# Kernel optimization log

Measured on AMD Instinct MI355X. Metric: run time of the kernel, lower is better.

Reference implementation:

```python
import jax, jax.numpy as jnp
import numpy as np

N = 100000
E = 1600000
F_IN = 256
H1, C1 = 8, 8          # conv1: 8 heads x 8 channels -> 64
H2, C2 = 1, 32         # conv2: 1 head x num_classes
SLOPE = 0.2


def gat_conv(x, src, dst, n, W, a_src, a_dst, b, heads, out):
    # x: [n, f_in]; W: [f_in, heads*out]; a_src/a_dst: [heads, out]; b: [heads*out]
    h = (x @ W).reshape(n, heads, out)                       # [n, H, C]
    s = jnp.sum(h * a_src, axis=-1)                          # [n, H]
    d = jnp.sum(h * a_dst, axis=-1)                          # [n, H]
    e = jax.nn.leaky_relu(s[src] + d[dst], SLOPE)            # [e, H]
    m = jax.ops.segment_max(e, dst, num_segments=n)          # stable segment softmax
    ex = jnp.exp(e - m[dst])
    z = jax.ops.segment_sum(ex, dst, num_segments=n)
    alpha = ex / (z[dst] + 1e-16)                            # [e, H]
    msg = alpha[:, :, None] * h[src]                         # [e, H, C]
    agg = jax.ops.segment_sum(msg, dst, num_segments=n)      # [n, H, C]
    return agg.reshape(n, heads * out) + b


def setup_inputs() -> dict:
    key = jax.random.key(0)
    ks = jax.random.split(key, 10)
    x = jax.random.normal(ks[0], (N, F_IN), dtype=jnp.float32)
    edge_index = jax.random.randint(ks[1], (2, E), 0, N, dtype=jnp.int32)
    sc = 0.05
    W1 = jax.random.normal(ks[2], (F_IN, H1 * C1), dtype=jnp.float32) * sc
    att_src1 = jax.random.normal(ks[3], (H1, C1), dtype=jnp.float32) * sc
    att_dst1 = jax.random.normal(ks[4], (H1, C1), dtype=jnp.float32) * sc
    b1 = jnp.zeros((H1 * C1,), dtype=jnp.float32)
    W2 = jax.random.normal(ks[5], (H1 * C1, H2 * C2), dtype=jnp.float32) * sc
    att_src2 = jax.random.normal(ks[6], (H2, C2), dtype=jnp.float32) * sc
    att_dst2 = jax.random.normal(ks[7], (H2, C2), dtype=jnp.float32) * sc
    b2 = jnp.zeros((H2 * C2,), dtype=jnp.float32)
    return {"x": x, "edge_index": edge_index, "W1": W1, "att_src1": att_src1,
            "att_dst1": att_dst1, "b1": b1, "W2": W2, "att_src2": att_src2,
            "att_dst2": att_dst2, "b2": b2}


def reference(x, edge_index, W1, att_src1, att_dst1, b1, W2, att_src2, att_dst2, b2):
    # add self loops (PyG GATConv default)
    loops = jnp.arange(N, dtype=edge_index.dtype)
    src = jnp.concatenate([edge_index[0], loops])
    dst = jnp.concatenate([edge_index[1], loops])
    # dropout layers are identity in eval mode
    h = gat_conv(x, src, dst, N, W1, att_src1, att_dst1, b1, H1, C1)
    h = jax.nn.elu(h)
    h = gat_conv(h, src, dst, N, W2, att_src2, att_dst2, b2, H2, C2)
    return jax.nn.log_softmax(h, axis=1)
```

## Files before the change

### kernel.cpp

```cpp
#include <hip/hip_runtime.h>
#include <hip/hip_bf16.h>

#define N_NODES 100000
#define N_EDGES 1600000
#define N_TOT   (N_EDGES + N_NODES)
#define F_IN    256
#define F1      64
#define H1      8
#define C1      8
#define F2      32
#define SLOPE   0.2f
#define CHUNK   2048
#define NCH     ((N_NODES + CHUNK - 1) / CHUNK)

#define NB_G    ((N_NODES + 255) / 256)
#define NB_H    ((N_EDGES + 255) / 256)

#define SLICES  8
#define SL_W    ((N_NODES + SLICES - 1) / SLICES)
#define CH_E    16384
#define NCHUNK  ((N_EDGES + CH_E - 1) / CH_E)

typedef unsigned int  uint;
typedef unsigned short ushort;
typedef __attribute__((ext_vector_type(8))) short bf16x8;
typedef __attribute__((ext_vector_type(4))) float f32x4;

__device__ inline ushort f2bf(float f) {
    uint u = __float_as_uint(f);
    uint r = u + 0x7fffu + ((u >> 16) & 1u);
    return (ushort)(r >> 16);
}
__device__ inline float bflo(uint u) { return __uint_as_float(u << 16); }
__device__ inline float bfhi(uint u) { return __uint_as_float(u & 0xffff0000u); }
__device__ inline uint pk2bf(float a, float b) {
    __hip_bfloat162 h = __float22bfloat162_rn(make_float2(a, b));
    union { __hip_bfloat162 h; uint u; } cv; cv.h = h;
    return cv.u;
}

__global__ __launch_bounds__(256) void k_gemm1_hist(
        const float* __restrict__ x, const float* __restrict__ W1,
        const float* __restrict__ as1, const float* __restrict__ ad1,
        const int* __restrict__ ei,
        ushort* __restrict__ h1b, float* __restrict__ s1, float* __restrict__ d1,
        int* __restrict__ cnt, int* __restrict__ rank) {
    __shared__ union {
        ushort B[F_IN * F1];
        ushort S[4][64][66];
    } sm;
    const int tid = threadIdx.x;

    if (blockIdx.x >= NB_G) {
        const int e = (blockIdx.x - NB_G) * 256 + tid;
        if (e < N_EDGES)
            rank[e] = atomicAdd(cnt + ei[N_EDGES + e], 1);
        return;
    }

    for (int i = 0; i < 64; ++i) {
        const int e = i * 256 + tid;
        const int k = e >> 6, n = e & 63;
        sm.B[((k >> 3) * 64 + n) * 8 + (k & 7)] = f2bf(W1[e]);
    }
    __syncthreads();

    const int wave = tid >> 6, lane = tid & 63;
    const int q = lane >> 4, ln = lane & 15;
    const int rowbase = blockIdx.x * 256 + wave * 64;

    f32x4 acc[4][4];
#pragma unroll
    for (int mt = 0; mt < 4; ++mt)
#pragma unroll
        for (int nt = 0; nt < 4; ++nt) acc[mt][nt] = (f32x4){0.f, 0.f, 0.f, 0.f};

    int rows[4];
#pragma unroll
    for (int mt = 0; mt < 4; ++mt) {
        const int r = rowbase + mt * 16 + ln;
        rows[mt] = r < N_NODES ? r : N_NODES - 1;
    }

    for (int t = 0; t < 8; ++t) {
        bf16x8 bfr[4];
#pragma unroll
        for (int nt = 0; nt < 4; ++nt)
            bfr[nt] = *(const bf16x8*)&sm.B[((t * 4 + q) * 64 + nt * 16 + ln) * 8];
#pragma unroll
        for (int mt = 0; mt < 4; ++mt) {
            const float4* ap = (const float4*)(x + (size_t)rows[mt] * F_IN + t * 32 + q * 8);
            const float4 a0 = ap[0], a1 = ap[1];
            uint4 au = make_uint4(pk2bf(a0.x, a0.y), pk2bf(a0.z, a0.w),
                                  pk2bf(a1.x, a1.y), pk2bf(a1.z, a1.w));
            bf16x8 af = *(bf16x8*)&au;
#pragma unroll
            for (int nt = 0; nt < 4; ++nt)
                acc[mt][nt] = __builtin_amdgcn_mfma_f32_16x16x32_bf16(
                                  af, bfr[nt], acc[mt][nt], 0, 0, 0);
        }
    }
    __syncthreads();

#pragma unroll
    for (int mt = 0; mt < 4; ++mt)
#pragma unroll
        for (int nt = 0; nt < 4; ++nt)
#pragma unroll
            for (int r = 0; r < 4; ++r)
                sm.S[wave][mt * 16 + q * 4 + r][nt * 16 + ln] = f2bf(acc[mt][nt][r]);
    __syncthreads();

    const int node = rowbase + lane;
    if (node >= N_NODES) return;
    const uint* srow = (const uint*)&sm.S[wave][lane][0];
    float sacc[H1], dacc[H1];
#pragma unroll
    for (int h = 0; h < H1; ++h) { sacc[h] = 0.f; dacc[h] = 0.f; }
    uint4* hout = (uint4*)(h1b + (size_t)node * F1);
#pragma unroll
    for (int p4 = 0; p4 < 8; ++p4) {
        const uint u0 = srow[p4 * 4 + 0], u1 = srow[p4 * 4 + 1];
        const uint u2 = srow[p4 * 4 + 2], u3 = srow[p4 * 4 + 3];
        hout[p4] = make_uint4(u0, u1, u2, u3);
        const float c[8] = {bflo(u0), bfhi(u0), bflo(u1), bfhi(u1),
                            bflo(u2), bfhi(u2), bflo(u3), bfhi(u3)};
#pragma unroll
        for (int j = 0; j < 8; ++j) {
            sacc[p4] += c[j] * as1[p4 * 8 + j];
            dacc[p4] += c[j] * ad1[p4 * 8 + j];
        }
    }
    float4* s4 = (float4*)(s1 + (size_t)node * H1);
    float4* d4 = (float4*)(d1 + (size_t)node * H1);
    s4[0] = make_float4(sacc[0], sacc[1], sacc[2], sacc[3]);
    s4[1] = make_float4(sacc[4], sacc[5], sacc[6], sacc[7]);
    d4[0] = make_float4(dacc[0], dacc[1], dacc[2], dacc[3]);
    d4[1] = make_float4(dacc[4], dacc[5], dacc[6], dacc[7]);
}

__global__ __launch_bounds__(256) void k_scan_a(
        const int* __restrict__ cnt, int* __restrict__ row_ptr,
        int* __restrict__ bsum) {
    __shared__ int sdata[256];
    const int tid = threadIdx.x;
    const int base = blockIdx.x * CHUNK + tid * 8;
    int v[8];
    int tot = 0;
#pragma unroll
    for (int j = 0; j < 8; ++j) {
        v[j] = (base + j < N_NODES) ? cnt[base + j] + 1 : 0;
        tot += v[j];
    }
    sdata[tid] = tot;
    __syncthreads();
    for (int off = 1; off < 256; off <<= 1) {
        int t = (tid >= off) ? sdata[tid - off] : 0;
        __syncthreads();
        sdata[tid] += t;
        __syncthreads();
    }
    int run = sdata[tid] - tot;
#pragma unroll
    for (int j = 0; j < 8; ++j) {
        if (base + j < N_NODES) row_ptr[base + j] = run;
        run += v[j];
    }
    if (tid == 255) bsum[blockIdx.x] = sdata[255];
}

__global__ __launch_bounds__(256) void k_scan_c2(
        int* __restrict__ row_ptr, const int* __restrict__ bsum,
        int* __restrict__ srcs) {
    __shared__ int pb[64];
    const int t = threadIdx.x;
    if (t < 64) {
        int v = (t < NCH) ? bsum[t] : 0;
        const int orig = v;
        for (int off = 1; off < 64; off <<= 1) {
            int u = __shfl_up(v, off);
            if (t >= off) v += u;
        }
        pb[t] = v - orig;
    }
    __syncthreads();
    const int i = blockIdx.x * 256 + t;
    if (i < N_NODES) {
        const int rp = row_ptr[i] + pb[i / CHUNK];
        row_ptr[i] = rp;
        srcs[rp] = i;
    } else if (i == N_NODES) row_ptr[N_NODES] = N_TOT;
}

__global__ __launch_bounds__(256) void k_scatter(
        const int* __restrict__ ei, const int* __restrict__ row_ptr,
        const int* __restrict__ rank, int* __restrict__ srcs) {
    const int slice = blockIdx.x % SLICES;
    const int chunk = blockIdx.x / SLICES;
    const int lo = slice * SL_W;
    const int base = chunk * CH_E;
    const int lim = (base + CH_E < N_EDGES) ? base + CH_E : N_EDGES;
    for (int i = base + threadIdx.x; i < lim; i += 256) {
        const int di = ei[N_EDGES + i];
        if ((uint)(di - lo) < (uint)SL_W)
            srcs[row_ptr[di] + 1 + rank[i]] = ei[i];
    }
}

__global__ __launch_bounds__(256) void k_agg1(
        const int* __restrict__ row_ptr, const int* __restrict__ srcs,
        const ushort* __restrict__ h1b, const float* __restrict__ s1,
        const float* __restrict__ d1, const float* __restrict__ b1,
        ushort* __restrict__ x2b) {
    const int wid = (blockIdx.x * 256 + threadIdx.x) >> 6;
    if (wid >= N_NODES) return;
    const int lane = threadIdx.x & 63;
    const int q = lane >> 4;
    const int c = lane & 15;
    const int hd = c >> 1;
    const float dh = d1[(size_t)wid * H1 + hd];
    const int beg = row_ptr[wid], end = row_ptr[wid + 1];
    const uint2* hv = (const uint2*)h1b;
    float a0 = 0.f, a1 = 0.f, a2 = 0.f, a3 = 0.f, z = 0.f;
    int i = beg + q;
    for (; i + 4 < end; i += 8) {
        const int sA = srcs[i], sB = srcs[i + 4];
        float eA = s1[(size_t)sA * H1 + hd] + dh;
        float eB = s1[(size_t)sB * H1 + hd] + dh;
        eA = eA > 0.f ? eA : SLOPE * eA;
        eB = eB > 0.f ? eB : SLOPE * eB;
        const float xA = __expf(eA), xB = __expf(eB);
        const uint2 UA = hv[(size_t)sA * 16 + c];
        const uint2 UB = hv[(size_t)sB * 16 + c];
        z  += xA + xB;
        a0 += xA * bflo(UA.x) + xB * bflo(UB.x);
        a1 += xA * bfhi(UA.x) + xB * bfhi(UB.x);
        a2 += xA * bflo(UA.y) + xB * bflo(UB.y);
        a3 += xA * bfhi(UA.y) + xB * bfhi(UB.y);
    }
    for (; i < end; i += 4) {
        const int sA = srcs[i];
        float eA = s1[(size_t)sA * H1 + hd] + dh;
        eA = eA > 0.f ? eA : SLOPE * eA;
        const float xA = __expf(eA);
        const uint2 UA = hv[(size_t)sA * 16 + c];
        z  += xA;
        a0 += xA * bflo(UA.x);
        a1 += xA * bfhi(UA.x);
        a2 += xA * bflo(UA.y);
        a3 += xA * bfhi(UA.y);
    }
#pragma unroll
    for (int off = 16; off <= 32; off <<= 1) {
        a0 += __shfl_xor(a0, off); a1 += __shfl_xor(a1, off);
        a2 += __shfl_xor(a2, off); a3 += __shfl_xor(a3, off);
        z  += __shfl_xor(z, off);
    }
    if (lane < 16) {
        const float zi = 1.f / (z + 1e-16f);
        float v0 = a0 * zi + b1[4 * c + 0];
        float v1 = a1 * zi + b1[4 * c + 1];
        float v2 = a2 * zi + b1[4 * c + 2];
        float v3 = a3 * zi + b1[4 * c + 3];
        v0 = v0 > 0.f ? v0 : __expf(v0) - 1.f;
        v1 = v1 > 0.f ? v1 : __expf(v1) - 1.f;
        v2 = v2 > 0.f ? v2 : __expf(v2) - 1.f;
        v3 = v3 > 0.f ? v3 : __expf(v3) - 1.f;
        ((uint2*)x2b)[(size_t)wid * 16 + c] = make_uint2(pk2bf(v0, v1), pk2bf(v2, v3));
    }
}

__global__ __launch_bounds__(256) void k_node1(
        const ushort* __restrict__ x2b, const float* __restrict__ W2,
        const float* __restrict__ as2, const float* __restrict__ ad2,
        ushort* __restrict__ h2b, float* __restrict__ s2, float* __restrict__ d2) {
    __shared__ float sW[F1 * F2];
    const int tid = threadIdx.x;
    const float4* W4 = (const float4*)W2;
    float4* sW4 = (float4*)sW;
#pragma unroll
    for (int i = 0; i < (F1 * F2 / 4) / 256; ++i)
        sW4[i * 256 + tid] = W4[i * 256 + tid];
    __syncthreads();

    const int n = blockIdx.x * 256 + tid;
    if (n >= N_NODES) return;

    float acc[F2];
#pragma unroll
    for (int c = 0; c < F2; ++c) acc[c] = 0.f;

    const uint4* xv4 = (const uint4*)(x2b + (size_t)n * F1);
#pragma unroll
    for (int q = 0; q < 8; ++q) {
        uint4 u = xv4[q];
        float xs[8] = {bflo(u.x), bfhi(u.x), bflo(u.y), bfhi(u.y),
                       bflo(u.z), bfhi(u.z), bflo(u.w), bfhi(u.w)};
#pragma unroll
        for (int kk = 0; kk < 8; ++kk) {
            const float t = xs[kk];
            const float4* wr = (const float4*)(sW + (q * 8 + kk) * F2);
#pragma unroll
            for (int c4 = 0; c4 < F2 / 4; ++c4) {
                float4 w = wr[c4];
                acc[c4 * 4 + 0] += t * w.x;
                acc[c4 * 4 + 1] += t * w.y;
                acc[c4 * 4 + 2] += t * w.z;
                acc[c4 * 4 + 3] += t * w.w;
            }
        }
    }

    uint up[F2 / 2];
#pragma unroll
    for (int j = 0; j < F2 / 2; ++j)
        up[j] = (uint)f2bf(acc[2 * j]) | ((uint)f2bf(acc[2 * j + 1]) << 16);
    uint4* o4 = (uint4*)(h2b + (size_t)n * F2);
#pragma unroll
    for (int q = 0; q < F2 / 8; ++q)
        o4[q] = make_uint4(up[q * 4 + 0], up[q * 4 + 1], up[q * 4 + 2], up[q * 4 + 3]);

    float s = 0.f, d = 0.f;
#pragma unroll
    for (int c = 0; c < F2; ++c) { s += acc[c] * as2[c]; d += acc[c] * ad2[c]; }
    s2[n] = s;
    d2[n] = d;
}

__global__ __launch_bounds__(256) void k_agg2(
        const int* __restrict__ row_ptr, const int* __restrict__ srcs,
        const ushort* __restrict__ h2b, const float* __restrict__ s2,
        const float* __restrict__ d2, const float* __restrict__ b2,
        float* __restrict__ out) {
    const int wid = (blockIdx.x * 256 + threadIdx.x) >> 6;
    if (wid >= N_NODES) return;
    const int lane = threadIdx.x & 63;
    const int q = lane >> 3;
    const int c = lane & 7;
    const float dn = d2[wid];
    const int beg = row_ptr[wid], end = row_ptr[wid + 1];
    const uint2* hv = (const uint2*)h2b;
    float a0 = 0.f, a1 = 0.f, a2 = 0.f, a3 = 0.f, z = 0.f;
    int i = beg + q;
    for (; i + 8 < end; i += 16) {
        const int sA = srcs[i], sB = srcs[i + 8];
        float eA = s2[sA] + dn;
        float eB = s2[sB] + dn;
        eA = eA > 0.f ? eA : SLOPE * eA;
        eB = eB > 0.f ? eB : SLOPE * eB;
        const float xA = __expf(eA), xB = __expf(eB);
        const uint2 UA = hv[(size_t)sA * 8 + c];
        const uint2 UB = hv[(size_t)sB * 8 + c];
        z  += xA + xB;
        a0 += xA * bflo(UA.x) + xB * bflo(UB.x);
        a1 += xA * bfhi(UA.x) + xB * bfhi(UB.x);
        a2 += xA * bflo(UA.y) + xB * bflo(UB.y);
        a3 += xA * bfhi(UA.y) + xB * bfhi(UB.y);
    }
    for (; i < end; i += 8) {
        const int sA = srcs[i];
        float eA = s2[sA] + dn;
        eA = eA > 0.f ? eA : SLOPE * eA;
        const float xA = __expf(eA);
        const uint2 UA = hv[(size_t)sA * 8 + c];
        z  += xA;
        a0 += xA * bflo(UA.x);
        a1 += xA * bfhi(UA.x);
        a2 += xA * bflo(UA.y);
        a3 += xA * bfhi(UA.y);
    }
#pragma unroll
    for (int off = 8; off <= 32; off <<= 1) {
        a0 += __shfl_xor(a0, off); a1 += __shfl_xor(a1, off);
        a2 += __shfl_xor(a2, off); a3 += __shfl_xor(a3, off);
        z  += __shfl_xor(z, off);
    }
    const float zi = 1.f / (z + 1e-16f);
    const float v0 = a0 * zi + b2[4 * c + 0];
    const float v1 = a1 * zi + b2[4 * c + 1];
    const float v2 = a2 * zi + b2[4 * c + 2];
    const float v3 = a3 * zi + b2[4 * c + 3];
    float m = fmaxf(fmaxf(v0, v1), fmaxf(v2, v3));
#pragma unroll
    for (int off = 1; off <= 4; off <<= 1) m = fmaxf(m, __shfl_xor(m, off));
    float ssum = __expf(v0 - m) + __expf(v1 - m) + __expf(v2 - m) + __expf(v3 - m);
#pragma unroll
    for (int off = 1; off <= 4; off <<= 1) ssum += __shfl_xor(ssum, off);
    const float lse = m + __logf(ssum);
    if (lane < 8)
        ((float4*)out)[(size_t)wid * 8 + c] =
            make_float4(v0 - lse, v1 - lse, v2 - lse, v3 - lse);
}

extern "C" void kernel_launch(void* const* d_in, const int* in_sizes, int n_in,
                              void* d_out, int out_size, void* d_ws, size_t ws_size,
                              hipStream_t stream) {
    const float* x   = (const float*)d_in[0];
    const int*   ei  = (const int*)d_in[1];
    const float* W1  = (const float*)d_in[2];
    const float* as1 = (const float*)d_in[3];
    const float* ad1 = (const float*)d_in[4];
    const float* b1  = (const float*)d_in[5];
    const float* W2  = (const float*)d_in[6];
    const float* as2 = (const float*)d_in[7];
    const float* ad2 = (const float*)d_in[8];
    const float* b2  = (const float*)d_in[9];
    float* out = (float*)d_out;

    ushort* h1b = (ushort*)d_ws;
    ushort* x2b = h1b + (size_t)N_NODES * F1;
    ushort* h2b = x2b + (size_t)N_NODES * F1;
    float*  s1  = (float*)(h2b + (size_t)N_NODES * F2);
    float*  d1  = s1 + (size_t)N_NODES * H1;
    float*  s2  = d1 + (size_t)N_NODES * H1;
    float*  d2  = s2 + N_NODES;
    int* cnt     = (int*)(d2 + N_NODES);
    int* rank    = cnt + N_NODES;
    int* row_ptr = rank + N_EDGES;
    int* bsum    = row_ptr + N_NODES + 1;
    int* srcs    = bsum + 64;

    hipMemsetAsync(cnt, 0, (size_t)N_NODES * sizeof(int), stream);

    const int nb_n = (N_NODES + 255) / 256;
    const int nb_w = (N_NODES * 64 + 255) / 256;

    k_gemm1_hist<<<NB_G + NB_H, 256, 0, stream>>>(x, W1, as1, ad1, ei,
                                                  h1b, s1, d1, cnt, rank);
    k_scan_a<<<NCH, 256, 0, stream>>>(cnt, row_ptr, bsum);
    k_scan_c2<<<(N_NODES + 256) / 256, 256, 0, stream>>>(row_ptr, bsum, srcs);
    k_scatter<<<SLICES * NCHUNK, 256, 0, stream>>>(ei, row_ptr, rank, srcs);
    k_agg1<<<nb_w, 256, 0, stream>>>(row_ptr, srcs, h1b, s1, d1, b1, x2b);
    k_node1<<<nb_n, 256, 0, stream>>>(x2b, W2, as2, ad2, h2b, s2, d2);
    k_agg2<<<nb_w, 256, 0, stream>>>(row_ptr, srcs, h2b, s2, d2, b2, out);
}
```

Baseline: 394.4 us.

## Fuse layer-2 linear transform and attention scores into layer-1 aggregation kernel

The separate k_node1 kernel is removed. Each wave in k_agg1 now stages its ELU output row in LDS and computes the 64x32 matvec with W2 read from global memory, then the s2/d2 dot products through wave shuffles. This drops the x2b bf16 round trip and one kernel launch. In exchange every wave re-reads W2 from global memory or cache instead of a block-shared LDS copy. The x2 row now feeds the matvec in fp32 instead of being rounded to bf16.

```diff
diff --git a/kernel.cpp b/kernel.cpp
--- a/kernel.cpp
+++ b/kernel.cpp
@@ -211,9 +211,14 @@
         const int* __restrict__ row_ptr, const int* __restrict__ srcs,
         const ushort* __restrict__ h1b, const float* __restrict__ s1,
         const float* __restrict__ d1, const float* __restrict__ b1,
-        ushort* __restrict__ x2b) {
+        const float* __restrict__ W2, const float* __restrict__ as2,
+        const float* __restrict__ ad2,
+        ushort* __restrict__ h2b, float* __restrict__ s2,
+        float* __restrict__ d2) {
+    __shared__ float sx[4][64];
     const int wid = (blockIdx.x * 256 + threadIdx.x) >> 6;
     if (wid >= N_NODES) return;
+    const int w = threadIdx.x >> 6;
     const int lane = threadIdx.x & 63;
     const int q = lane >> 4;
     const int c = lane & 15;
@@ -266,65 +271,32 @@
         v1 = v1 > 0.f ? v1 : __expf(v1) - 1.f;
         v2 = v2 > 0.f ? v2 : __expf(v2) - 1.f;
         v3 = v3 > 0.f ? v3 : __expf(v3) - 1.f;
-        ((uint2*)x2b)[(size_t)wid * 16 + c] = make_uint2(pk2bf(v0, v1), pk2bf(v2, v3));
-    }
-}
-
-__global__ __launch_bounds__(256) void k_node1(
-        const ushort* __restrict__ x2b, const float* __restrict__ W2,
-        const float* __restrict__ as2, const float* __restrict__ ad2,
-        ushort* __restrict__ h2b, float* __restrict__ s2, float* __restrict__ d2) {
-    __shared__ float sW[F1 * F2];
-    const int tid = threadIdx.x;
-    const float4* W4 = (const float4*)W2;
-    float4* sW4 = (float4*)sW;
-#pragma unroll
-    for (int i = 0; i < (F1 * F2 / 4) / 256; ++i)
-        sW4[i * 256 + tid] = W4[i * 256 + tid];
-    __syncthreads();
-
-    const int n = blockIdx.x * 256 + tid;
-    if (n >= N_NODES) return;
-
-    float acc[F2];
-#pragma unroll
-    for (int c = 0; c < F2; ++c) acc[c] = 0.f;
-
-    const uint4* xv4 = (const uint4*)(x2b + (size_t)n * F1);
-#pragma unroll
-    for (int q = 0; q < 8; ++q) {
-        uint4 u = xv4[q];
-        float xs[8] = {bflo(u.x), bfhi(u.x), bflo(u.y), bfhi(u.y),
-                       bflo(u.z), bfhi(u.z), bflo(u.w), bfhi(u.w)};
-#pragma unroll
-        for (int kk = 0; kk < 8; ++kk) {
-            const float t = xs[kk];
-            const float4* wr = (const float4*)(sW + (q * 8 + kk) * F2);
-#pragma unroll
-            for (int c4 = 0; c4 < F2 / 4; ++c4) {
-                float4 w = wr[c4];
-                acc[c4 * 4 + 0] += t * w.x;
-                acc[c4 * 4 + 1] += t * w.y;
-                acc[c4 * 4 + 2] += t * w.z;
-                acc[c4 * 4 + 3] += t * w.w;
-            }
-        }
-    }
-
-    uint up[F2 / 2];
-#pragma unroll
-    for (int j = 0; j < F2 / 2; ++j)
-        up[j] = (uint)f2bf(acc[2 * j]) | ((uint)f2bf(acc[2 * j + 1]) << 16);
-    uint4* o4 = (uint4*)(h2b + (size_t)n * F2);
-#pragma unroll
-    for (int q = 0; q < F2 / 8; ++q)
-        o4[q] = make_uint4(up[q * 4 + 0], up[q * 4 + 1], up[q * 4 + 2], up[q * 4 + 3]);
-
-    float s = 0.f, d = 0.f;
-#pragma unroll
-    for (int c = 0; c < F2; ++c) { s += acc[c] * as2[c]; d += acc[c] * ad2[c]; }
-    s2[n] = s;
-    d2[n] = d;
+        *(float4*)&sx[w][4 * lane] = make_float4(v0, v1, v2, v3);
+    }
+    __builtin_amdgcn_wave_barrier();
+
+    const int kh = lane >> 5;
+    const int oc = lane & 31;
+    const float4* sxv = (const float4*)&sx[w][kh * 32];
+    const float* wp0 = W2 + (size_t)(kh * 32) * F2 + oc;
+    float acc = 0.f;
+#pragma unroll
+    for (int k4 = 0; k4 < 8; ++k4) {
+        const float4 xv = sxv[k4];
+        const float* wp = wp0 + (size_t)k4 * 4 * F2;
+        acc += xv.x * wp[0]      + xv.y * wp[F2]
+             + xv.z * wp[2 * F2] + xv.w * wp[3 * F2];
+    }
+    acc += __shfl_xor(acc, 32);
+
+    float sA2 = acc * as2[oc], dA2 = acc * ad2[oc];
+#pragma unroll
+    for (int off = 1; off <= 16; off <<= 1) {
+        sA2 += __shfl_xor(sA2, off);
+        dA2 += __shfl_xor(dA2, off);
+    }
+    if (lane < 32) h2b[(size_t)wid * F2 + oc] = f2bf(acc);
+    if (lane == 0) { s2[wid] = sA2; d2[wid] = dA2; }
 }
 
 __global__ __launch_bounds__(256) void k_agg2(
@@ -408,8 +380,7 @@
     float* out = (float*)d_out;
 
     ushort* h1b = (ushort*)d_ws;
-    ushort* x2b = h1b + (size_t)N_NODES * F1;
-    ushort* h2b = x2b + (size_t)N_NODES * F1;
+    ushort* h2b = h1b + (size_t)N_NODES * F1;
     float*  s1  = (float*)(h2b + (size_t)N_NODES * F2);
     float*  d1  = s1 + (size_t)N_NODES * H1;
     float*  s2  = d1 + (size_t)N_NODES * H1;
@@ -422,7 +393,6 @@
 
     hipMemsetAsync(cnt, 0, (size_t)N_NODES * sizeof(int), stream);
 
-    const int nb_n = (N_NODES + 255) / 256;
     const int nb_w = (N_NODES * 64 + 255) / 256;
 
     k_gemm1_hist<<<NB_G + NB_H, 256, 0, stream>>>(x, W1, as1, ad1, ei,
@@ -430,7 +400,7 @@
     k_scan_a<<<NCH, 256, 0, stream>>>(cnt, row_ptr, bsum);
     k_scan_c2<<<(N_NODES + 256) / 256, 256, 0, stream>>>(row_ptr, bsum, srcs);
     k_scatter<<<SLICES * NCHUNK, 256, 0, stream>>>(ei, row_ptr, rank, srcs);
-    k_agg1<<<nb_w, 256, 0, stream>>>(row_ptr, srcs, h1b, s1, d1, b1, x2b);
-    k_node1<<<nb_n, 256, 0, stream>>>(x2b, W2, as2, ad2, h2b, s2, d2);
+    k_agg1<<<nb_w, 256, 0, stream>>>(row_ptr, srcs, h1b, s1, d1, b1,
+                                     W2, as2, ad2, h2b, s2, d2);
     k_agg2<<<nb_w, 256, 0, stream>>>(row_ptr, srcs, h2b, s2, d2, b2, out);
 }
```

Result: no change. 399.9 us (+1.4%).
